# Performance work log

Hardware: AMD Instinct MI355X
Metric: run time of the kernel (lower is better)

Reference implementation:

```python
import jax, jax.numpy as jnp
import numpy as np

C = 768
H = 12
HD = C // H  # 64


def setup_inputs() -> dict:
    key = jax.random.key(0)
    k1, k2, k3, k4, k5, k6 = jax.random.split(key, 6)
    B, T = 8, 1024
    x = jax.random.normal(k1, (B, T, C), dtype=jnp.float32)
    mask = jax.random.randint(k2, (B, T), 0, 2, dtype=jnp.int32)
    # Linear params stored so that y = x @ W + b (W is [in, out])
    W_attn = jax.random.normal(k3, (C, 3 * C), dtype=jnp.float32) * 0.02
    b_attn = jax.random.normal(k4, (3 * C,), dtype=jnp.float32) * 0.02
    W_proj = jax.random.normal(k5, (C, C), dtype=jnp.float32) * 0.02
    b_proj = jax.random.normal(k6, (C,), dtype=jnp.float32) * 0.02
    return {"x": x, "mask": mask, "W_attn": W_attn, "b_attn": b_attn,
            "W_proj": W_proj, "b_proj": b_proj}


def reference(x, mask, W_attn, b_attn, W_proj, b_proj):
    B, T, _ = x.shape
    qkv = x @ W_attn + b_attn                      # [B, T, 3C]
    q, k, v = jnp.split(qkv, 3, axis=2)            # each [B, T, C]
    # [B, T, C] -> [B, H, T, HD]
    q = q.reshape(B, T, H, HD).transpose(0, 2, 1, 3)
    k = k.reshape(B, T, H, HD).transpose(0, 2, 1, 3)
    v = v.reshape(B, T, H, HD).transpose(0, 2, 1, 3)

    scale = 1.0 / np.sqrt(HD).astype(np.float32)
    att = jnp.einsum('bhqd,bhkd->bhqk', q, k) * scale  # [B, H, T, T]

    causal = jnp.tril(jnp.ones((T, T), dtype=bool))    # [T, T]
    att = jnp.where(causal[None, None], att, -jnp.inf)

    # custom mask: per-(batch, query-row) flag; where mask==0 the whole row
    # of scores is overwritten with 0.0001 (AFTER causal fill, as in torch)
    row_masked = (mask == 0)[:, None, :, None]         # [B, 1, T, 1]
    att = jnp.where(row_masked, jnp.float32(1e-4), att)

    att = jax.nn.softmax(att, axis=-1)
    # dropout layers are identity in eval mode
    y = jnp.einsum('bhqk,bhkd->bhqd', att, v)          # [B, H, T, HD]
    y = y.transpose(0, 2, 1, 3).reshape(B, T, C)
    y = y @ W_proj + b_proj
    return y
```

## Files before the change

kernel.cpp:

```cpp
#include <hip/hip_runtime.h>

#define BQ 8
#define TT 1024
#define CC 768
#define NH 12
#define HD 64
#define BH (BQ*NH)
#define MROWS (BQ*TT)
#define NQKV (3*CC)
#define KD CC

typedef unsigned short u16;
typedef __attribute__((ext_vector_type(4))) short short4v;
typedef __attribute__((ext_vector_type(8))) short short8v;
typedef __attribute__((ext_vector_type(4))) float floatx4;
typedef __attribute__((address_space(1))) const unsigned int gu32;
typedef __attribute__((address_space(3))) unsigned int lu32;

__device__ __forceinline__ float bf2f(u16 u) {
  union { unsigned int i; float f; } c; c.i = ((unsigned int)u) << 16; return c.f;
}
__device__ __forceinline__ u16 f2bf(float f) {
  union { float f; unsigned int i; } c; c.f = f;
  unsigned int i = c.i;
  return (u16)((i + 0x7FFFu + ((i >> 16) & 1u)) >> 16);
}
__device__ __forceinline__ float fast_exp2(float x) {
  return __builtin_amdgcn_exp2f(x);
}
__device__ __forceinline__ void async_ld16(const u16* g, u16* l) {
  __builtin_amdgcn_global_load_lds((gu32*)g, (lu32*)l, 16, 0, 0);
}

__global__ __launch_bounds__(256) void convert_f32_bf16(
    const float* __restrict__ in, u16* __restrict__ out, int n)
{
  int i = (blockIdx.x * 256 + threadIdx.x) * 4;
  if (i >= n) return;
  floatx4 v = *(const floatx4*)(in + i);
  short4v o;
  o[0] = (short)f2bf(v[0]); o[1] = (short)f2bf(v[1]);
  o[2] = (short)f2bf(v[2]); o[3] = (short)f2bf(v[3]);
  *(short4v*)(out + i) = o;
}

__global__ __launch_bounds__(256) void transpose_f32_bf16(
    const float* __restrict__ in, u16* __restrict__ out, int R, int Cc)
{
  __shared__ float tile[32][33];
  int ct = Cc >> 5;
  int bx = blockIdx.x % ct;
  int by = blockIdx.x / ct;
  int tx = threadIdx.x & 31;
  int ty = threadIdx.x >> 5;
  int c0 = bx << 5, r0 = by << 5;
#pragma unroll
  for (int s = 0; s < 4; ++s)
    tile[ty + s*8][tx] = in[(size_t)(r0 + ty + s*8) * Cc + c0 + tx];
  __syncthreads();
#pragma unroll
  for (int s = 0; s < 4; ++s)
    out[(size_t)(c0 + ty + s*8) * R + r0 + tx] = f2bf(tile[tx][ty + s*8]);
}

__global__ __launch_bounds__(256) void gemm_bt(
    const u16* __restrict__ A, const u16* __restrict__ Bt,
    const float* __restrict__ bias,
    float* __restrict__ out,
    u16* __restrict__ qo, u16* __restrict__ ko, u16* __restrict__ vo,
    int M, int N, int mode)
{
  __shared__ u16 As[64 * 64];
  __shared__ u16 Bs[128 * 64];

  int tid = threadIdx.x;
  int lane = tid & 63;
  int w = tid >> 6;
  int c = lane & 15;
  int q4 = lane >> 4;

  int mtiles = M >> 6;
  int mt = blockIdx.x % mtiles;
  int nt = blockIdx.x / mtiles;
  int m0 = mt << 6, n0 = nt << 7;

  int wr = (w >> 1) << 5;
  int wc = (w & 1) << 6;

  int srow8 = lane >> 3;
  int ug = ((lane & 7) ^ srow8) << 3;
  const u16* ag = A  + (size_t)(m0 + w * 16 + srow8) * KD + ug;
  const u16* bg = Bt + (size_t)(n0 + w * 32 + srow8) * KD + ug;
  u16* asl = &As[(w * 16) * 64];
  u16* bsl = &Bs[(w * 32) * 64];

  floatx4 acc[2][4];
#pragma unroll
  for (int mi = 0; mi < 2; ++mi)
#pragma unroll
    for (int ni = 0; ni < 4; ++ni) acc[mi][ni] = (floatx4){0.f, 0.f, 0.f, 0.f};

  int c7 = c & 7;

#pragma unroll 1
  for (int kt = 0; kt < KD; kt += 64) {
    async_ld16(ag + kt,              asl);
    async_ld16(ag + kt + 8 * KD,     asl + 8 * 64);
    async_ld16(bg + kt,              bsl);
    async_ld16(bg + kt + 8 * KD,     bsl + 8 * 64);
    async_ld16(bg + kt + 16 * KD,    bsl + 16 * 64);
    async_ld16(bg + kt + 24 * KD,    bsl + 24 * 64);
    __syncthreads();

    short8v af[2][2], bf[4][2];
#pragma unroll
    for (int kc = 0; kc < 2; ++kc) {
      int uoff = ((kc * 4 + q4) ^ c7) << 3;
#pragma unroll
      for (int mi = 0; mi < 2; ++mi)
        af[mi][kc] = *(const short8v*)&As[(wr + mi * 16 + c) * 64 + uoff];
#pragma unroll
      for (int ni = 0; ni < 4; ++ni)
        bf[ni][kc] = *(const short8v*)&Bs[(wc + ni * 16 + c) * 64 + uoff];
    }
#pragma unroll
    for (int kc = 0; kc < 2; ++kc)
#pragma unroll
      for (int mi = 0; mi < 2; ++mi)
#pragma unroll
        for (int ni = 0; ni < 4; ++ni)
          acc[mi][ni] = __builtin_amdgcn_mfma_f32_16x16x32_bf16(af[mi][kc], bf[ni][kc], acc[mi][ni], 0, 0, 0);
    __syncthreads();
  }

  if (mode == 0) {
    int which = (n0 + wc) / CC;
    int nbase = (n0 + wc) - which * CC;
    u16* dst0 = (which == 0) ? qo : ((which == 1) ? ko : vo);
#pragma unroll
    for (int ni = 0; ni < 4; ++ni) {
      int nn = nbase + ni * 16 + c;
      int hh = nn >> 6, dd = nn & 63;
      float bv = bias[which * CC + nn];
#pragma unroll
      for (int mi = 0; mi < 2; ++mi) {
#pragma unroll
        for (int r = 0; r < 4; ++r) {
          int mm = m0 + wr + mi * 16 + q4 * 4 + r;
          int bb = mm >> 10, tt = mm & 1023;
          size_t idx = (((size_t)(bb * NH + hh)) * TT + tt) * HD + dd;
          dst0[idx] = f2bf(acc[mi][ni][r] + bv);
        }
      }
    }
  } else {
#pragma unroll
    for (int ni = 0; ni < 4; ++ni) {
      int nn = n0 + wc + ni * 16 + c;
      float bv = bias[nn];
#pragma unroll
      for (int mi = 0; mi < 2; ++mi) {
#pragma unroll
        for (int r = 0; r < 4; ++r) {
          int mm = m0 + wr + mi * 16 + q4 * 4 + r;
          out[(size_t)mm * N + nn] = acc[mi][ni][r] + bv;
        }
      }
    }
  }
}

__global__ __launch_bounds__(256) void transpose_v(
    const u16* __restrict__ vb, u16* __restrict__ vt)
{
  __shared__ u16 tile[64][72];
  int tid = threadIdx.x;
  int tt0 = (blockIdx.x & 15) << 6;
  int bh = blockIdx.x >> 4;
  {
    int trow = tid >> 2;
    int dchunk = (tid & 3) << 4;
    const u16* src = vb + (((size_t)bh * TT + tt0 + trow) * HD) + dchunk;
    *(short8v*)&tile[trow][dchunk]     = *(const short8v*)src;
    *(short8v*)&tile[trow][dchunk + 8] = *(const short8v*)(src + 8);
  }
  __syncthreads();
  {
    int drow = tid >> 2;
    int tchunk = (tid & 3) << 4;
    short8v a, bv;
#pragma unroll
    for (int j = 0; j < 8; ++j) {
      a[j]  = (short)tile[tchunk + j][drow];
      bv[j] = (short)tile[tchunk + 8 + j][drow];
    }
    u16* dst = vt + ((size_t)bh * HD + drow) * TT + tt0 + tchunk;
    *(short8v*)dst       = a;
    *(short8v*)(dst + 8) = bv;
  }
}

__global__ __launch_bounds__(64) void vmean_kernel(
    const u16* __restrict__ vb, float* __restrict__ mv)
{
  int bh = blockIdx.x;
  int d = threadIdx.x;
  const u16* p = vb + (size_t)bh * TT * HD + d;
  float s0 = 0.f, s1 = 0.f, s2 = 0.f, s3 = 0.f;
  for (int t = 0; t < TT; t += 4) {
    s0 += bf2f(p[(size_t)(t + 0) * HD]);
    s1 += bf2f(p[(size_t)(t + 1) * HD]);
    s2 += bf2f(p[(size_t)(t + 2) * HD]);
    s3 += bf2f(p[(size_t)(t + 3) * HD]);
  }
  mv[bh * HD + d] = (s0 + s1 + s2 + s3) * (1.0f / 1024.0f);
}

#define LDW 72
#define SCL 0.18033688f

__global__ __launch_bounds__(256) void attn_kernel(
    const u16* __restrict__ qb, const u16* __restrict__ kb,
    const u16* __restrict__ vtb, const int* __restrict__ mask,
    const float* __restrict__ meanv, u16* __restrict__ outb)
{
  __shared__ u16 Ks[64 * LDW];
  __shared__ u16 Vs[64 * LDW];
  __shared__ u16 Ps[4][16 * LDW];

  int tid = threadIdx.x;
  int lane = tid & 63;
  int w = tid >> 6;
  int c = lane & 15;
  int q4 = lane >> 4;

  int pair = blockIdx.x & 7;
  int bh = blockIdx.x >> 3;
  int b = bh / NH;
  int h = bh - b * NH;

  int srow = tid >> 2;
  int schunk = (tid & 3) << 4;
  const u16* kgp = kb + ((size_t)bh * TT + srow) * HD + schunk;
  const u16* vgp = vtb + ((size_t)bh * HD + srow) * TT + schunk;
  u16* ksw = &Ks[srow * LDW + schunk];
  u16* vsw = &Vs[srow * LDW + schunk];
  u16* pw = &Ps[w][0];

#pragma unroll 1
  for (int phase = 0; phase < 2; ++phase) {
    int qt = phase ? (15 - pair) : pair;
    int rowbase = (qt << 6) + (w << 4);

    short8v qfrag[2];
    {
      const u16* qp = qb + ((size_t)bh * TT + rowbase + c) * HD + q4 * 8;
      qfrag[0] = *(const short8v*)qp;
      qfrag[1] = *(const short8v*)(qp + 32);
    }

    floatx4 o[4];
#pragma unroll
    for (int i = 0; i < 4; ++i) o[i] = (floatx4){0.f, 0.f, 0.f, 0.f};
    float m_i[4], l_i[4];
#pragma unroll
    for (int r = 0; r < 4; ++r) { m_i[r] = -INFINITY; l_i[r] = 0.f; }

    short8v kr0, kr1, vr0, vr1;
    kr0 = *(const short8v*)kgp;
    kr1 = *(const short8v*)(kgp + 8);
    vr0 = *(const short8v*)vgp;
    vr1 = *(const short8v*)(vgp + 8);

#pragma unroll 1
    for (int kt = 0; kt <= qt; ++kt) {
      __syncthreads();
      *(short8v*)ksw = kr0; *(short8v*)(ksw + 8) = kr1;
      *(short8v*)vsw = vr0; *(short8v*)(vsw + 8) = vr1;
      __syncthreads();

      if (kt < qt) {
        const u16* kp = kgp + ((size_t)(kt + 1) << 6) * HD;
        const u16* vp = vgp + ((kt + 1) << 6);
        kr0 = *(const short8v*)kp;
        kr1 = *(const short8v*)(kp + 8);
        vr0 = *(const short8v*)vp;
        vr1 = *(const short8v*)(vp + 8);
      }

      floatx4 s[4];
#pragma unroll
      for (int nt = 0; nt < 4; ++nt) s[nt] = (floatx4){0.f, 0.f, 0.f, 0.f};
#pragma unroll
      for (int kc = 0; kc < 2; ++kc) {
#pragma unroll
        for (int nt = 0; nt < 4; ++nt) {
          short8v kf = *(const short8v*)&Ks[(nt * 16 + c) * LDW + kc * 32 + q4 * 8];
          s[nt] = __builtin_amdgcn_mfma_f32_16x16x32_bf16(qfrag[kc], kf, s[nt], 0, 0, 0);
        }
      }

      if (kt == qt) {
#pragma unroll
        for (int nt = 0; nt < 4; ++nt)
#pragma unroll
          for (int r = 0; r < 4; ++r) {
            float sv = s[nt][r] * SCL;
            if (nt * 16 + c > (w << 4) + q4 * 4 + r) sv = -INFINITY;
            s[nt][r] = sv;
          }
      } else {
#pragma unroll
        for (int nt = 0; nt < 4; ++nt)
#pragma unroll
          for (int r = 0; r < 4; ++r) s[nt][r] *= SCL;
      }

      float mt[4];
#pragma unroll
      for (int r = 0; r < 4; ++r)
        mt[r] = fmaxf(fmaxf(s[0][r], s[1][r]), fmaxf(s[2][r], s[3][r]));
#pragma unroll
      for (int r = 0; r < 4; ++r) {
        mt[r] = fmaxf(mt[r], __shfl_xor(mt[r], 1));
        mt[r] = fmaxf(mt[r], __shfl_xor(mt[r], 2));
        mt[r] = fmaxf(mt[r], __shfl_xor(mt[r], 4));
        mt[r] = fmaxf(mt[r], __shfl_xor(mt[r], 8));
      }

      float al[4];
#pragma unroll
      for (int r = 0; r < 4; ++r) {
        float mn = fmaxf(m_i[r], mt[r]);
        al[r] = fast_exp2(m_i[r] - mn);
        m_i[r] = mn;
      }

      float ps[4] = {0.f, 0.f, 0.f, 0.f};
#pragma unroll
      for (int nt = 0; nt < 4; ++nt)
#pragma unroll
        for (int r = 0; r < 4; ++r) {
          float p = fast_exp2(s[nt][r] - m_i[r]);
          ps[r] += p;
          pw[(q4 * 4 + r) * LDW + nt * 16 + c] = f2bf(p);
        }
#pragma unroll
      for (int r = 0; r < 4; ++r) {
        ps[r] += __shfl_xor(ps[r], 1);
        ps[r] += __shfl_xor(ps[r], 2);
        ps[r] += __shfl_xor(ps[r], 4);
        ps[r] += __shfl_xor(ps[r], 8);
        l_i[r] = l_i[r] * al[r] + ps[r];
      }
#pragma unroll
      for (int nt = 0; nt < 4; ++nt)
#pragma unroll
        for (int r = 0; r < 4; ++r) o[nt][r] *= al[r];

#pragma unroll
      for (int kc = 0; kc < 2; ++kc) {
        short8v pf = *(const short8v*)&pw[c * LDW + kc * 32 + q4 * 8];
#pragma unroll
        for (int nt = 0; nt < 4; ++nt) {
          short8v vf = *(const short8v*)&Vs[(nt * 16 + c) * LDW + kc * 32 + q4 * 8];
          o[nt] = __builtin_amdgcn_mfma_f32_16x16x32_bf16(pf, vf, o[nt], 0, 0, 0);
        }
      }
    }

    int qrow[4]; bool msk[4]; float inv[4];
#pragma unroll
    for (int r = 0; r < 4; ++r) {
      qrow[r] = rowbase + q4 * 4 + r;
      msk[r] = (mask[b * TT + qrow[r]] == 0);
      inv[r] = 1.f / l_i[r];
    }
#pragma unroll
    for (int nt = 0; nt < 4; ++nt) {
      int d = nt * 16 + c;
      float mv = meanv[bh * HD + d];
#pragma unroll
      for (int r = 0; r < 4; ++r) {
        float val = msk[r] ? mv : o[nt][r] * inv[r];
        outb[((size_t)(b * TT + qrow[r])) * CC + h * HD + d] = f2bf(val);
      }
    }
  }
}

extern "C" void kernel_launch(void* const* d_in, const int* in_sizes, int n_in,
                              void* d_out, int out_size, void* d_ws, size_t ws_size,
                              hipStream_t stream)
{
  (void)in_sizes; (void)n_in; (void)out_size; (void)ws_size;
  const float* x     = (const float*)d_in[0];
  const int*   mask  = (const int*)d_in[1];
  const float* Wattn = (const float*)d_in[2];
  const float* battn = (const float*)d_in[3];
  const float* Wproj = (const float*)d_in[4];
  const float* bproj = (const float*)d_in[5];
  float* out = (float*)d_out;

  char* ws = (char*)d_ws;
  size_t off = 0;
  auto alloc = [&](size_t bytes) -> void* {
    void* p = ws + off;
    off += (bytes + 255) & ~(size_t)255;
    return p;
  };
  u16* WtA  = (u16*)alloc((size_t)NQKV * KD * 2);
  u16* WtP  = (u16*)alloc((size_t)CC * CC * 2);
  u16* xb   = (u16*)alloc((size_t)MROWS * CC * 2);
  u16* qbuf = (u16*)alloc((size_t)MROWS * CC * 2);
  u16* kbuf = (u16*)alloc((size_t)MROWS * CC * 2);
  u16* vbuf = (u16*)alloc((size_t)MROWS * CC * 2);
  u16* vtb  = (u16*)alloc((size_t)MROWS * CC * 2);
  u16* abuf = (u16*)alloc((size_t)MROWS * CC * 2);
  float* mv = (float*)alloc((size_t)BH * HD * 4);

  int nx = MROWS * CC;
  convert_f32_bf16<<<nx / (256 * 4), 256, 0, stream>>>(x, xb, nx);
  transpose_f32_bf16<<<(NQKV/32)*(KD/32), 256, 0, stream>>>(Wattn, WtA, KD, NQKV);
  transpose_f32_bf16<<<(CC/32)*(CC/32),   256, 0, stream>>>(Wproj, WtP, CC, CC);

  gemm_bt<<<(MROWS/64)*(NQKV/128), 256, 0, stream>>>(
      xb, WtA, battn, nullptr, qbuf, kbuf, vbuf, MROWS, NQKV, 0);

  transpose_v<<<BH * (TT/64), 256, 0, stream>>>(vbuf, vtb);
  vmean_kernel<<<BH, 64, 0, stream>>>(vbuf, mv);

  attn_kernel<<<BH * 8, 256, 0, stream>>>(qbuf, kbuf, vtb, mask, mv, abuf);

  gemm_bt<<<(MROWS/64)*(CC/128), 256, 0, stream>>>(
      abuf, WtP, bproj, out, nullptr, nullptr, nullptr, MROWS, CC, 1);
}
```

Before: 218.5 us.

## Replace online softmax max with Cauchy-Schwarz bound and MFMA row sums

Adds a kernel that computes, for each batch-head, the largest key L2 norm. The attention kernel then uses |q|·max|k|·scale as a fixed per-row softmax shift instead of a running maximum. This removes the per-tile max reductions, cross-lane shuffles, exp rescale factors and accumulator rescaling. Row sums of P are now produced by an extra MFMA against a vector of ones rather than by shuffle reductions. The cost is one small extra launch, plus a risk of exp underflow (and division by zero) when the norm bound is far above the true maximum score.

```diff
diff --git a/kernel.cpp b/kernel.cpp
--- a/kernel.cpp
+++ b/kernel.cpp
@@ -216,13 +216,45 @@
   mv[bh * HD + d] = (s0 + s1 + s2 + s3) * (1.0f / 1024.0f);
 }
 
+__global__ __launch_bounds__(256) void knorm_kernel(
+    const u16* __restrict__ kb, float* __restrict__ kmaxn)
+{
+  __shared__ float red[256];
+  int bh = blockIdx.x;
+  int tid = threadIdx.x;
+  float mx = 0.f;
+#pragma unroll 1
+  for (int t = tid; t < TT; t += 256) {
+    const u16* p = kb + ((size_t)bh * TT + t) * HD;
+    float s = 0.f;
+#pragma unroll
+    for (int j = 0; j < 64; j += 8) {
+      short8v v = *(const short8v*)(p + j);
+#pragma unroll
+      for (int i = 0; i < 8; ++i) {
+        float f = bf2f((u16)v[i]);
+        s = fmaf(f, f, s);
+      }
+    }
+    mx = fmaxf(mx, s);
+  }
+  red[tid] = mx;
+  __syncthreads();
+  for (int s2 = 128; s2 > 0; s2 >>= 1) {
+    if (tid < s2) red[tid] = fmaxf(red[tid], red[tid + s2]);
+    __syncthreads();
+  }
+  if (tid == 0) kmaxn[bh] = sqrtf(red[0]);
+}
+
 #define LDW 72
 #define SCL 0.18033688f
 
 __global__ __launch_bounds__(256) void attn_kernel(
     const u16* __restrict__ qb, const u16* __restrict__ kb,
     const u16* __restrict__ vtb, const int* __restrict__ mask,
-    const float* __restrict__ meanv, u16* __restrict__ outb)
+    const float* __restrict__ meanv, const float* __restrict__ kmaxn,
+    u16* __restrict__ outb)
 {
   __shared__ u16 Ks[64 * LDW];
   __shared__ u16 Vs[64 * LDW];
@@ -238,6 +270,7 @@
   int bh = blockIdx.x >> 3;
   int b = bh / NH;
   int h = bh - b * NH;
+  float kmax = kmaxn[bh];
 
   int srow = tid >> 2;
   int schunk = (tid & 3) << 4;
@@ -247,6 +280,10 @@
   u16* vsw = &Vs[srow * LDW + schunk];
   u16* pw = &Ps[w][0];
 
+  short8v onesv;
+#pragma unroll
+  for (int j = 0; j < 8; ++j) onesv[j] = (short)0x3F80;
+
 #pragma unroll 1
   for (int phase = 0; phase < 2; ++phase) {
     int qt = phase ? (15 - pair) : pair;
@@ -259,12 +296,25 @@
       qfrag[1] = *(const short8v*)(qp + 32);
     }
 
+    float q2 = 0.f;
+#pragma unroll
+    for (int kc = 0; kc < 2; ++kc)
+#pragma unroll
+      for (int j = 0; j < 8; ++j) {
+        float qv = bf2f((u16)qfrag[kc][j]);
+        q2 = fmaf(qv, qv, q2);
+      }
+    q2 += __shfl_xor(q2, 16);
+    q2 += __shfl_xor(q2, 32);
+    float Mc = sqrtf(q2) * kmax * SCL;
+    float Mrow[4];
+#pragma unroll
+    for (int r = 0; r < 4; ++r) Mrow[r] = __shfl(Mc, (q4 << 2) + r);
+
     floatx4 o[4];
 #pragma unroll
     for (int i = 0; i < 4; ++i) o[i] = (floatx4){0.f, 0.f, 0.f, 0.f};
-    float m_i[4], l_i[4];
-#pragma unroll
-    for (int r = 0; r < 4; ++r) { m_i[r] = -INFINITY; l_i[r] = 0.f; }
+    floatx4 o5 = (floatx4){0.f, 0.f, 0.f, 0.f};
 
     short8v kr0, kr1, vr0, vr1;
     kr0 = *(const short8v*)kgp;
@@ -305,58 +355,20 @@
         for (int nt = 0; nt < 4; ++nt)
 #pragma unroll
           for (int r = 0; r < 4; ++r) {
-            float sv = s[nt][r] * SCL;
+            float sv = s[nt][r];
             if (nt * 16 + c > (w << 4) + q4 * 4 + r) sv = -INFINITY;
-            s[nt][r] = sv;
+            float p = fast_exp2(fmaf(sv, SCL, -Mrow[r]));
+            pw[(q4 * 4 + r) * LDW + nt * 16 + c] = f2bf(p);
           }
       } else {
 #pragma unroll
         for (int nt = 0; nt < 4; ++nt)
 #pragma unroll
-          for (int r = 0; r < 4; ++r) s[nt][r] *= SCL;
-      }
-
-      float mt[4];
-#pragma unroll
-      for (int r = 0; r < 4; ++r)
-        mt[r] = fmaxf(fmaxf(s[0][r], s[1][r]), fmaxf(s[2][r], s[3][r]));
-#pragma unroll
-      for (int r = 0; r < 4; ++r) {
-        mt[r] = fmaxf(mt[r], __shfl_xor(mt[r], 1));
-        mt[r] = fmaxf(mt[r], __shfl_xor(mt[r], 2));
-        mt[r] = fmaxf(mt[r], __shfl_xor(mt[r], 4));
-        mt[r] = fmaxf(mt[r], __shfl_xor(mt[r], 8));
-      }
-
-      float al[4];
-#pragma unroll
-      for (int r = 0; r < 4; ++r) {
-        float mn = fmaxf(m_i[r], mt[r]);
-        al[r] = fast_exp2(m_i[r] - mn);
-        m_i[r] = mn;
-      }
-
-      float ps[4] = {0.f, 0.f, 0.f, 0.f};
-#pragma unroll
-      for (int nt = 0; nt < 4; ++nt)
-#pragma unroll
-        for (int r = 0; r < 4; ++r) {
-          float p = fast_exp2(s[nt][r] - m_i[r]);
-          ps[r] += p;
-          pw[(q4 * 4 + r) * LDW + nt * 16 + c] = f2bf(p);
-        }
-#pragma unroll
-      for (int r = 0; r < 4; ++r) {
-        ps[r] += __shfl_xor(ps[r], 1);
-        ps[r] += __shfl_xor(ps[r], 2);
-        ps[r] += __shfl_xor(ps[r], 4);
-        ps[r] += __shfl_xor(ps[r], 8);
-        l_i[r] = l_i[r] * al[r] + ps[r];
-      }
-#pragma unroll
-      for (int nt = 0; nt < 4; ++nt)
-#pragma unroll
-        for (int r = 0; r < 4; ++r) o[nt][r] *= al[r];
+          for (int r = 0; r < 4; ++r) {
+            float p = fast_exp2(fmaf(s[nt][r], SCL, -Mrow[r]));
+            pw[(q4 * 4 + r) * LDW + nt * 16 + c] = f2bf(p);
+          }
+      }
 
 #pragma unroll
       for (int kc = 0; kc < 2; ++kc) {
@@ -366,6 +378,7 @@
           short8v vf = *(const short8v*)&Vs[(nt * 16 + c) * LDW + kc * 32 + q4 * 8];
           o[nt] = __builtin_amdgcn_mfma_f32_16x16x32_bf16(pf, vf, o[nt], 0, 0, 0);
         }
+        o5 = __builtin_amdgcn_mfma_f32_16x16x32_bf16(pf, onesv, o5, 0, 0, 0);
       }
     }
 
@@ -374,7 +387,7 @@
     for (int r = 0; r < 4; ++r) {
       qrow[r] = rowbase + q4 * 4 + r;
       msk[r] = (mask[b * TT + qrow[r]] == 0);
-      inv[r] = 1.f / l_i[r];
+      inv[r] = 1.f / o5[r];
     }
 #pragma unroll
     for (int nt = 0; nt < 4; ++nt) {
@@ -418,6 +431,7 @@
   u16* vtb  = (u16*)alloc((size_t)MROWS * CC * 2);
   u16* abuf = (u16*)alloc((size_t)MROWS * CC * 2);
   float* mv = (float*)alloc((size_t)BH * HD * 4);
+  float* kmx = (float*)alloc((size_t)BH * 4);
 
   int nx = MROWS * CC;
   convert_f32_bf16<<<nx / (256 * 4), 256, 0, stream>>>(x, xb, nx);
@@ -429,8 +443,9 @@
 
   transpose_v<<<BH * (TT/64), 256, 0, stream>>>(vbuf, vtb);
   vmean_kernel<<<BH, 64, 0, stream>>>(vbuf, mv);
-
-  attn_kernel<<<BH * 8, 256, 0, stream>>>(qbuf, kbuf, vtb, mask, mv, abuf);
+  knorm_kernel<<<BH, 256, 0, stream>>>(kbuf, kmx);
+
+  attn_kernel<<<BH * 8, 256, 0, stream>>>(qbuf, kbuf, vtb, mask, mv, kmx, abuf);
 
   gemm_bt<<<(MROWS/64)*(CC/128), 256, 0, stream>>>(
       abuf, WtP, bproj, out, nullptr, nullptr, nullptr, MROWS, CC, 1);
```

New measurement: 214.2 us. -2.0%, faster.
